# Kernel tuning notes

Hardware: AMD Instinct MI355X
Metric: run time of the kernel (lower is better)

Reference implementation:

```python
import jax, jax.numpy as jnp
import numpy as np


def _closest_dist_sum(p1, p2):
    # p1: [B, N, 3], p2: [B, M, 3]
    # Euclidean distance via the expanded quadratic form; matches
    # torch.norm(p1 - p2, 2, dim=3) -> min over p2 -> sum over all.
    d2 = (jnp.sum(p1 * p1, axis=-1)[:, :, None]
          + jnp.sum(p2 * p2, axis=-1)[:, None, :]
          - 2.0 * jnp.einsum('bnd,bmd->bnm', p1, p2))  # [B, N, M]
    d = jnp.sqrt(jnp.maximum(d2, 0.0))
    return jnp.sum(jnp.min(d, axis=2))


def setup_inputs() -> dict:
    key = jax.random.key(0)
    k1, k2 = jax.random.split(key)
    shape_xyz = jax.random.normal(k1, (8, 8192, 6), dtype=jnp.float32)
    skel_xyz = jax.random.normal(k2, (8, 2048, 3), dtype=jnp.float32)
    return {"shape_xyz": shape_xyz, "skel_xyz": skel_xyz}


def reference(shape_xyz, skel_xyz):
    # normals (shape_xyz[:, :, 3:6]) are extracted but unused in the loss
    pts = shape_xyz[:, :, :3]
    cd1 = _closest_dist_sum(pts, skel_xyz)   # shape -> skeleton
    cd2 = _closest_dist_sum(skel_xyz, pts)   # skeleton -> shape
    loss_cd = (cd1 + cd2) * 0.0001
    return loss_cd
```

## Files before the change

### kernel.cpp

```cpp
#include <hip/hip_runtime.h>

#define BATCH   8
#define SHAPE_N 8192
#define SKEL_M  2048

#define WS2_OFF 512
#define CNT_OFF 66048
#define RED_OFF 66056
#define SKC_OFF 66176
#define SHC_OFF (66176 + 131072)

typedef short bf16x8 __attribute__((ext_vector_type(8)));
typedef float f32x16 __attribute__((ext_vector_type(16)));
union FragU { bf16x8 v; uint4 u4; };

__device__ __forceinline__ unsigned int f2bf(float a) {
    unsigned int u = __float_as_uint(a);
    return (u + 0x7FFFu + ((u >> 16) & 1u)) >> 16;
}
__device__ __forceinline__ float bf2f(unsigned int h) {
    return __uint_as_float(h << 16);
}
__device__ __forceinline__ unsigned int pack2(unsigned int lo, unsigned int hi) {
    return lo | (hi << 16);
}
__device__ __forceinline__ void bfsplit(float v, unsigned int& h, unsigned int& l) {
    h = f2bf(v);
    l = f2bf(v - bf2f(h));
}

__device__ __forceinline__ void conv_point(float bx, float by, float bz,
                                           uint4& hi, uint4& lo) {
    const float cx = -2.f * bx, cy = -2.f * by, cz = -2.f * bz;
    const float rb = bx * bx + by * by + bz * bz;
    unsigned int chx, clx, chy, cly, chz, clz, rbh, rbl;
    bfsplit(cx, chx, clx); bfsplit(cy, chy, cly); bfsplit(cz, chz, clz);
    bfsplit(rb, rbh, rbl);
    hi = make_uint4(pack2(chx, chy), pack2(chz, rbh),
                    pack2(chx, chy), pack2(chz, rbl));
    lo = make_uint4(pack2(clx, cly), pack2(clz, 0u), 0u, 0u);
}

__global__ __launch_bounds__(256) void cd_prep(
    const float* __restrict__ shape, const float* __restrict__ skel,
    float* __restrict__ ws)
{
    if (blockIdx.x == 0 && threadIdx.x == 0)
        ((int*)ws)[CNT_OFF] = 0;

    const int p = blockIdx.x * 256 + threadIdx.x;
    const float* q;
    uint4* dst;
    int idx;
    if (p < BATCH * SKEL_M) {
        const int b = p >> 11; idx = p & (SKEL_M - 1);
        q = skel + (size_t)p * 3;
        dst = (uint4*)(ws + SKC_OFF) + (size_t)b * 4096;
    } else {
        const int s = p - BATCH * SKEL_M;
        const int b = s >> 13; idx = s & (SHAPE_N - 1);
        q = shape + (size_t)s * 6;
        dst = (uint4*)(ws + SHC_OFF) + (size_t)b * 16384;
    }
    uint4 hi, lo;
    conv_point(q[0], q[1], q[2], hi, lo);
    const int g = idx >> 5, r = idx & 31;
    dst[g * 64 + r]      = hi;
    dst[g * 64 + 32 + r] = lo;
}

__device__ __forceinline__ void step_min(const FragU& af, const FragU* bf,
                                         float* rmin)
{
    const f32x16 Z = {0,0,0,0,0,0,0,0,0,0,0,0,0,0,0,0};
#pragma unroll
    for (int j = 0; j < 4; ++j) {
        f32x16 D = __builtin_amdgcn_mfma_f32_32x32x16_bf16(
            af.v, bf[j].v, Z, 0, 0, 0);
        const float t0 = fminf(fminf(D[0],  D[1]),  D[2]);
        const float t1 = fminf(fminf(D[3],  D[4]),  D[5]);
        const float t2 = fminf(fminf(D[6],  D[7]),  D[8]);
        const float t3 = fminf(fminf(D[9],  D[10]), D[11]);
        const float t4 = fminf(fminf(D[12], D[13]), D[14]);
        const float u0 = fminf(fminf(t0, t1), t2);
        const float u1 = fminf(fminf(t3, t4), D[15]);
        rmin[j] = fminf(rmin[j], fminf(u0, u1));
    }
}

template <int SA>
__device__ __forceinline__ void cd_scan2(
    const float* __restrict__ Araw,
    const uint4* __restrict__ Bconv,
    float* rmin, float* ra)
{
    const int tid = threadIdx.x;
    const int l = tid & 63, wv = tid >> 6;
    const unsigned int one = 0x3F80u;

    FragU bf[4];
#pragma unroll
    for (int j = 0; j < 4; ++j) {
        const float* p = Araw + (size_t)(j * 32 + (l & 31)) * SA;
        const float x = p[0], y = p[1], z = p[2];
        ra[j] = x * x + y * y + z * z;
        unsigned int hx, lx, hy, ly, hz, lz;
        bfsplit(x, hx, lx); bfsplit(y, hy, ly); bfsplit(z, hz, lz);
        if (l < 32)
            bf[j].u4 = make_uint4(pack2(hx, hy), pack2(hz, one),
                                  pack2(lx, ly), pack2(lz, one));
        else
            bf[j].u4 = make_uint4(pack2(hx, hy), pack2(hz, 0u), 0u, 0u);
        rmin[j] = 3.4e38f;
    }

    const char* p0 = (const char*)Bconv + wv * 16384 +
                     (l >> 5) * 512 + (l & 31) * 16;

    FragU f[8];
#pragma unroll
    for (int g = 0; g < 8; ++g)
        f[g].u4 = *(const uint4*)(p0 + g * 1024);
#pragma unroll
    for (int g = 0; g < 8; ++g) {
        const FragU cur = f[g];
        f[g].u4 = *(const uint4*)(p0 + (g + 8) * 1024);
        step_min(cur, bf, rmin);
    }
#pragma unroll
    for (int g = 0; g < 8; ++g)
        step_min(f[g], bf, rmin);

#pragma unroll
    for (int j = 0; j < 4; ++j)
        rmin[j] = fminf(rmin[j], __shfl_xor(rmin[j], 32, 64));
}

__global__ __launch_bounds__(256, 4) void cd_main(
    const float* __restrict__ shape, const float* __restrict__ skel,
    float* __restrict__ ws)
{
    __shared__ float smin[4][128];
    __shared__ float sra[128];
    __shared__ float s_wsum[2];
    const int tid = threadIdx.x;
    const int l = tid & 63, wv = tid >> 6;
    const int bid = (blockIdx.x & 7) * 128 + (blockIdx.x >> 3);
    float rmin[4], ra[4];

    if (bid < 512) {
        const int b = bid >> 6, sub = bid & 63;
        cd_scan2<6>(shape + ((size_t)b * SHAPE_N + sub * 128) * 6,
                    (const uint4*)(ws + SKC_OFF) + (size_t)b * 4096,
                    rmin, ra);
    } else {
        const int j = bid - 512;
        const int b = j >> 6, rem = j & 63;
        const int asub = rem >> 2, bs = rem & 3;
        cd_scan2<3>(skel + ((size_t)b * SKEL_M + asub * 128) * 3,
                    (const uint4*)(ws + SHC_OFF) + (size_t)b * 16384 + bs * 4096,
                    rmin, ra);
    }

    if (l < 32) {
#pragma unroll
        for (int j = 0; j < 4; ++j) smin[wv][j * 32 + l] = rmin[j];
        if (wv == 0) {
#pragma unroll
            for (int j = 0; j < 4; ++j) sra[j * 32 + l] = ra[j];
        }
    }
    __syncthreads();

    if (bid < 512) {
        float d = 0.f;
        if (tid < 128) {
            const float m = fminf(fminf(smin[0][tid], smin[1][tid]),
                                  fminf(smin[2][tid], smin[3][tid]));
            d = sqrtf(fmaxf(sra[tid] + m, 0.f));
        }
        for (int o = 32; o; o >>= 1) d += __shfl_down(d, o, 64);
        if (l == 0 && wv < 2) s_wsum[wv] = d;
        __syncthreads();
        if (tid == 0) ws[bid] = s_wsum[0] + s_wsum[1];
    } else {
        if (tid < 128) {
            const int j = bid - 512;
            const int b = j >> 6, rem = j & 63;
            const int asub = rem >> 2, bs = rem & 3;
            const float m = fminf(fminf(smin[0][tid], smin[1][tid]),
                                  fminf(smin[2][tid], smin[3][tid]));
            ws[WS2_OFF + bs * (BATCH * SKEL_M) + b * SKEL_M +
               asub * 128 + tid] = sra[tid] + m;
        }
    }
}

__global__ __launch_bounds__(256) void cd_reduce(
    float* __restrict__ ws, float* __restrict__ out)
{
    __shared__ float s_wsum[4];
    __shared__ int s_last;
    const int t = threadIdx.x;
    const int bid = blockIdx.x;
    const int l = t & 63, wv = t >> 6;
    const int i = bid * 256 + t;

    const float v0 = ws[WS2_OFF + i];
    const float v1 = ws[WS2_OFF + 16384 + i];
    const float v2 = ws[WS2_OFF + 32768 + i];
    const float v3 = ws[WS2_OFF + 49152 + i];
    float s = sqrtf(fmaxf(fminf(fminf(v0, v1), fminf(v2, v3)), 0.f));
    if (bid < 2) s += ws[bid * 256 + t];

    for (int o = 32; o; o >>= 1) s += __shfl_down(s, o, 64);
    if (l == 0) s_wsum[wv] = s;
    __syncthreads();
    if (t == 0) {
        ws[RED_OFF + bid] = s_wsum[0] + s_wsum[1] + s_wsum[2] + s_wsum[3];
        __threadfence();
        const int old = atomicAdd((int*)ws + CNT_OFF, 1);
        s_last = (old == 63);
    }
    __syncthreads();
    if (s_last && wv == 0) {
        __threadfence();
        float f = ws[RED_OFF + l];
        for (int o = 32; o; o >>= 1) f += __shfl_down(f, o, 64);
        if (l == 0) out[0] = f * 1e-4f;
    }
}

extern "C" void kernel_launch(void* const* d_in, const int* in_sizes, int n_in,
                              void* d_out, int out_size, void* d_ws, size_t ws_size,
                              hipStream_t stream) {
    const float* shape = (const float*)d_in[0];
    const float* skel  = (const float*)d_in[1];
    float* out         = (float*)d_out;
    float* ws          = (float*)d_ws;

    cd_prep<<<320, 256, 0, stream>>>(shape, skel, ws);
    cd_main<<<1024, 256, 0, stream>>>(shape, skel, ws);
    cd_reduce<<<64, 256, 0, stream>>>(ws, out);
}
```

Measured before the change: 72.71 us.

## Double per-block A tile to 256 points, halving grid and B-fragment reloads

Each block now holds 8 A-side MFMA fragments (256 query points) instead of 4, so every loaded B fragment feeds twice as many MFMAs and total B traffic is halved. The grid drops from 1024 to 512 blocks, launch bounds go from 4 to 2 blocks per SM, and the shared-memory reduction and output indexing are adjusted to match. The trade-off is higher register pressure and fewer blocks to spread over 256 CUs, which may reduce occupancy and latency hiding.

```diff
diff --git a/kernel.cpp b/kernel.cpp
--- a/kernel.cpp
+++ b/kernel.cpp
@@ -69,12 +69,12 @@
     dst[g * 64 + 32 + r] = lo;
 }
 
-__device__ __forceinline__ void step_min(const FragU& af, const FragU* bf,
-                                         float* rmin)
+__device__ __forceinline__ void step_min8(const FragU& af, const FragU* bf,
+                                          float* rmin)
 {
     const f32x16 Z = {0,0,0,0,0,0,0,0,0,0,0,0,0,0,0,0};
 #pragma unroll
-    for (int j = 0; j < 4; ++j) {
+    for (int j = 0; j < 8; ++j) {
         f32x16 D = __builtin_amdgcn_mfma_f32_32x32x16_bf16(
             af.v, bf[j].v, Z, 0, 0, 0);
         const float t0 = fminf(fminf(D[0],  D[1]),  D[2]);
@@ -89,7 +89,7 @@
 }
 
 template <int SA>
-__device__ __forceinline__ void cd_scan2(
+__device__ __forceinline__ void cd_scan8(
     const float* __restrict__ Araw,
     const uint4* __restrict__ Bconv,
     float* rmin, float* ra)
@@ -98,9 +98,9 @@
     const int l = tid & 63, wv = tid >> 6;
     const unsigned int one = 0x3F80u;
 
-    FragU bf[4];
-#pragma unroll
-    for (int j = 0; j < 4; ++j) {
+    FragU bf[8];
+#pragma unroll
+    for (int j = 0; j < 8; ++j) {
         const float* p = Araw + (size_t)(j * 32 + (l & 31)) * SA;
         const float x = p[0], y = p[1], z = p[2];
         ra[j] = x * x + y * y + z * z;
@@ -125,74 +125,68 @@
     for (int g = 0; g < 8; ++g) {
         const FragU cur = f[g];
         f[g].u4 = *(const uint4*)(p0 + (g + 8) * 1024);
-        step_min(cur, bf, rmin);
+        step_min8(cur, bf, rmin);
     }
 #pragma unroll
     for (int g = 0; g < 8; ++g)
-        step_min(f[g], bf, rmin);
-
-#pragma unroll
-    for (int j = 0; j < 4; ++j)
+        step_min8(f[g], bf, rmin);
+
+#pragma unroll
+    for (int j = 0; j < 8; ++j)
         rmin[j] = fminf(rmin[j], __shfl_xor(rmin[j], 32, 64));
 }
 
-__global__ __launch_bounds__(256, 4) void cd_main(
+__global__ __launch_bounds__(256, 2) void cd_main(
     const float* __restrict__ shape, const float* __restrict__ skel,
     float* __restrict__ ws)
 {
-    __shared__ float smin[4][128];
-    __shared__ float sra[128];
-    __shared__ float s_wsum[2];
+    __shared__ float smin[4][256];
+    __shared__ float sra[256];
+    __shared__ float s_wsum[4];
     const int tid = threadIdx.x;
     const int l = tid & 63, wv = tid >> 6;
-    const int bid = (blockIdx.x & 7) * 128 + (blockIdx.x >> 3);
-    float rmin[4], ra[4];
-
-    if (bid < 512) {
-        const int b = bid >> 6, sub = bid & 63;
-        cd_scan2<6>(shape + ((size_t)b * SHAPE_N + sub * 128) * 6,
+    const int bid = (blockIdx.x & 7) * 64 + (blockIdx.x >> 3);
+    float rmin[8], ra[8];
+
+    if (bid < 256) {
+        const int b = bid >> 5, asub = bid & 31;
+        cd_scan8<6>(shape + ((size_t)b * SHAPE_N + asub * 256) * 6,
                     (const uint4*)(ws + SKC_OFF) + (size_t)b * 4096,
                     rmin, ra);
     } else {
-        const int j = bid - 512;
-        const int b = j >> 6, rem = j & 63;
+        const int j = bid - 256;
+        const int b = j >> 5, rem = j & 31;
         const int asub = rem >> 2, bs = rem & 3;
-        cd_scan2<3>(skel + ((size_t)b * SKEL_M + asub * 128) * 3,
+        cd_scan8<3>(skel + ((size_t)b * SKEL_M + asub * 256) * 3,
                     (const uint4*)(ws + SHC_OFF) + (size_t)b * 16384 + bs * 4096,
                     rmin, ra);
     }
 
     if (l < 32) {
 #pragma unroll
-        for (int j = 0; j < 4; ++j) smin[wv][j * 32 + l] = rmin[j];
+        for (int j = 0; j < 8; ++j) smin[wv][j * 32 + l] = rmin[j];
         if (wv == 0) {
 #pragma unroll
-            for (int j = 0; j < 4; ++j) sra[j * 32 + l] = ra[j];
+            for (int j = 0; j < 8; ++j) sra[j * 32 + l] = ra[j];
         }
     }
     __syncthreads();
 
-    if (bid < 512) {
-        float d = 0.f;
-        if (tid < 128) {
-            const float m = fminf(fminf(smin[0][tid], smin[1][tid]),
-                                  fminf(smin[2][tid], smin[3][tid]));
-            d = sqrtf(fmaxf(sra[tid] + m, 0.f));
-        }
+    const float m = fminf(fminf(smin[0][tid], smin[1][tid]),
+                          fminf(smin[2][tid], smin[3][tid]));
+    if (bid < 256) {
+        float d = sqrtf(fmaxf(sra[tid] + m, 0.f));
         for (int o = 32; o; o >>= 1) d += __shfl_down(d, o, 64);
-        if (l == 0 && wv < 2) s_wsum[wv] = d;
+        if (l == 0) s_wsum[wv] = d;
         __syncthreads();
-        if (tid == 0) ws[bid] = s_wsum[0] + s_wsum[1];
+        if (tid == 0)
+            ws[bid] = s_wsum[0] + s_wsum[1] + s_wsum[2] + s_wsum[3];
     } else {
-        if (tid < 128) {
-            const int j = bid - 512;
-            const int b = j >> 6, rem = j & 63;
-            const int asub = rem >> 2, bs = rem & 3;
-            const float m = fminf(fminf(smin[0][tid], smin[1][tid]),
-                                  fminf(smin[2][tid], smin[3][tid]));
-            ws[WS2_OFF + bs * (BATCH * SKEL_M) + b * SKEL_M +
-               asub * 128 + tid] = sra[tid] + m;
-        }
+        const int j = bid - 256;
+        const int b = j >> 5, rem = j & 31;
+        const int asub = rem >> 2, bs = rem & 3;
+        ws[WS2_OFF + bs * (BATCH * SKEL_M) + b * SKEL_M +
+           asub * 256 + tid] = sra[tid] + m;
     }
 }
 
@@ -211,7 +205,7 @@
     const float v2 = ws[WS2_OFF + 32768 + i];
     const float v3 = ws[WS2_OFF + 49152 + i];
     float s = sqrtf(fmaxf(fminf(fminf(v0, v1), fminf(v2, v3)), 0.f));
-    if (bid < 2) s += ws[bid * 256 + t];
+    if (bid == 0) s += ws[t];
 
     for (int o = 32; o; o >>= 1) s += __shfl_down(s, o, 64);
     if (l == 0) s_wsum[wv] = s;
@@ -240,6 +234,6 @@
     float* ws          = (float*)d_ws;
 
     cd_prep<<<320, 256, 0, stream>>>(shape, skel, ws);
-    cd_main<<<1024, 256, 0, stream>>>(shape, skel, ws);
+    cd_main<<<512, 256, 0, stream>>>(shape, skel, ws);
     cd_reduce<<<64, 256, 0, stream>>>(ws, out);
 }
```

Measured after the change: 73.32 us. Within noise of the previous version (+0.8%).
